# Optimization experiments

Measured on AMD Instinct MI355X. Metric: run time of the kernel, lower is better.

The kernel has to match this reference:

```python
import jax, jax.numpy as jnp
import numpy as np

B, D, M_CONS = 512, 1024, 256
TOL = 0.01          # projection_tolerance
ROUNDS = 3
RHO0 = 3.0          # step
XRHO0 = 0.5         # forward() default xrho
FACTOR = 1.0
MAX_ITER = 30       # cap on the (originally unbounded) Dykstra while-loop


def setup_inputs() -> dict:
    key = jax.random.key(0)
    k1, k2, k3, k4, k5 = jax.random.split(key, 5)
    A = jax.random.normal(k1, (M_CONS, D), jnp.float32) / np.float32(np.sqrt(D))
    # feasible b so the polyhedron {Ax=b, x>=0} is nonempty and Dykstra converges
    x_feas = jax.nn.relu(jax.random.normal(k2, (D,), jnp.float32))
    b = A @ x_feas                                  # [M_CONS]
    AA = A.T @ jnp.linalg.inv(A @ A.T)              # [D, M_CONS], precomputed as in __init__
    c = jax.random.normal(k3, (B, D), jnp.float32)
    L = jax.random.normal(k4, (D, D), jnp.float32)
    Lam = 1.0 + 0.1 * jax.random.normal(k5, (D,), jnp.float32)
    return {"c": c, "A": A, "b": b, "AA": AA, "L": L, "Lam": Lam}


def reference(c, A, b, AA, L, Lam):
    # step matrix: L @ diag(Lam) @ inv(L)   (recomputed identically each round in torch)
    M = (L * Lam[None, :]) @ jnp.linalg.inv(L)      # [D, D]

    def proj(x):  # affine projection onto {Ax = b}: (x.T - AA @ (A x.T - b)).T
        return x - (x @ A.T - b[None, :]) @ AA.T    # [B, D]

    def project_pol(x0):  # Dykstra alternating projection onto {Ax=b} n {x>=0}
        def body(carry, _):
            x, p, q, y_out, done = carry
            y = proj(x + p)
            err = jnp.max(jax.nn.relu(-y))
            y_out = jnp.where(done, y_out, y)       # freeze output at first convergence
            xn = jax.nn.relu(y + q)
            pn = x + p - y
            qn = y + q - xn
            sel = lambda old, new: jnp.where(done, old, new)
            new_done = done | (err < TOL)
            return (sel(x, xn), sel(p, pn), sel(q, qn), y_out, new_done), None

        z = jnp.zeros_like(x0)
        init = (x0, z, z, x0, jnp.array(False))
        (xf, pf, qf, y_out, d), _ = jax.lax.scan(body, init, None, length=MAX_ITER)
        return y_out

    x = jnp.zeros_like(c)
    rho, xrho = RHO0, XRHO0
    for _ in range(ROUNDS):
        x = x - (xrho * (x @ M.T) + rho * c)
        x = project_pol(x)
        rho = rho * FACTOR
        xrho = xrho * FACTOR
    return x
```

## Files before the change

kernel.cpp:

```cpp
#include <hip/hip_runtime.h>

#define D      1024
#define BSZ    512
#define MC     256
#define NBK    64
#define NPAN   16
#define N_ROUNDS 3
#define MAXIT  30
#define TOLV   0.01f
#define RHOV   3.0f
#define XRHOV  0.5f
#define GRID   256
#define NGA    128
#define NGB    128

#define TS   0
#define QS   4096
#define US   8192
#define PART 9216
#define BS   13312
#define RED  13568
#define SMF  13600

struct KArgs {
  const float *c, *A, *b, *AA, *L, *Lam;
  float *yout, *F, *Ybuf, *Wm;
  float *t, *At, *AAt;
  int *perm, *rmap;
  unsigned *slotsF, *slotsG, *errb;
};

__device__ __forceinline__ void fbar(unsigned* slots, int lid, int count, unsigned target) {
  __syncthreads();
  if (threadIdx.x == 0) {
    __builtin_amdgcn_fence(__ATOMIC_RELEASE, "agent");
    __hip_atomic_store(&slots[lid * 16], target, __ATOMIC_RELAXED, __HIP_MEMORY_SCOPE_AGENT);
  }
  for (int i = threadIdx.x; i < count; i += 256)
    while (__hip_atomic_load(&slots[i * 16], __ATOMIC_RELAXED, __HIP_MEMORY_SCOPE_AGENT) < target)
      __builtin_amdgcn_s_sleep(1);
  __builtin_amdgcn_fence(__ATOMIC_ACQUIRE, "agent");
  __syncthreads();
}

__device__ __forceinline__ void tile_fma(const float (*As)[68], const float (*Bs)[68],
                                         float acc[4][4], const int tx, const int ty) {
#pragma unroll 8
  for (int kk = 0; kk < 64; ++kk) {
    const float4 a4 = *(const float4*)(&As[kk][ty * 4]);
    const float4 b4 = *(const float4*)(&Bs[kk][tx * 4]);
    const float a0 = a4.x, a1 = a4.y, a2 = a4.z, a3 = a4.w;
    const float b0 = b4.x, b1 = b4.y, b2 = b4.z, b3 = b4.w;
    acc[0][0] = fmaf(a0, b0, acc[0][0]); acc[0][1] = fmaf(a0, b1, acc[0][1]);
    acc[0][2] = fmaf(a0, b2, acc[0][2]); acc[0][3] = fmaf(a0, b3, acc[0][3]);
    acc[1][0] = fmaf(a1, b0, acc[1][0]); acc[1][1] = fmaf(a1, b1, acc[1][1]);
    acc[1][2] = fmaf(a1, b2, acc[1][2]); acc[1][3] = fmaf(a1, b3, acc[1][3]);
    acc[2][0] = fmaf(a2, b0, acc[2][0]); acc[2][1] = fmaf(a2, b1, acc[2][1]);
    acc[2][2] = fmaf(a2, b2, acc[2][2]); acc[2][3] = fmaf(a2, b3, acc[2][3]);
    acc[3][0] = fmaf(a3, b0, acc[3][0]); acc[3][1] = fmaf(a3, b1, acc[3][1]);
    acc[3][2] = fmaf(a3, b2, acc[3][2]); acc[3][3] = fmaf(a3, b3, acc[3][3]);
  }
}

__device__ void ph_prep(float* sm, int vb, const float* L, const float* Lam,
                        float* F, float* Ybuf) {
  float (*tile)[65] = (float(*)[65])sm;
  const int bi = vb >> 4, bj = vb & 15;
  const int tx = threadIdx.x & 63, ty4 = threadIdx.x >> 6;
  const int i0 = bi * 64, j0 = bj * 64;
  for (int r = ty4; r < 64; r += 4) {
    const float v = L[(size_t)(i0 + r) * D + j0 + tx];
    F[(size_t)(i0 + r) * D + j0 + tx] = v;
    tile[r][tx] = v;
  }
  __syncthreads();
  for (int r = ty4; r < 64; r += 4) {
    const int j = j0 + r;
    Ybuf[(size_t)j * D + i0 + tx] = Lam[j] * tile[tx][r];
  }
  __syncthreads();
}

__device__ void ph_transpose(float* sm, const float* src, float* dst,
                             int srows, int scols, int tr, int tc) {
  float (*tile)[65] = (float(*)[65])sm;
  const int tx = threadIdx.x & 63, ty = threadIdx.x >> 6;
  for (int r = ty; r < 64; r += 4)
    tile[r][tx] = src[(size_t)(tr * 64 + r) * scols + tc * 64 + tx];
  __syncthreads();
  for (int r = ty; r < 64; r += 4)
    dst[(size_t)(tc * 64 + r) * srows + tr * 64 + tx] = tile[tx][r];
  __syncthreads();
}

__device__ void ph_lu_diag(float* sm, float* F, int* perm, int* rmap, int k) {
  float (*blk)[65] = (float(*)[65])sm;
  int* pr_sh = (int*)&sm[8960];
  int* rmp   = (int*)&sm[8964];
  const int tid = threadIdx.x;
  const int c0 = k * NBK;
  for (int e = tid; e < 4096; e += 256) {
    const int r = e >> 6, c = e & 63;
    blk[r][c] = F[(size_t)(c0 + r) * D + c0 + c];
  }
  if (tid < 64) rmp[tid] = tid;
  __syncthreads();
  for (int j = 0; j < 64; ++j) {
    if (tid < 64) {
      float v = (tid >= j) ? fabsf(blk[tid][j]) : -1.0f;
      int ridx = tid;
      for (int off = 32; off > 0; off >>= 1) {
        const float ov = __shfl_down(v, off);
        const int oi = __shfl_down(ridx, off);
        if (ov > v) { v = ov; ridx = oi; }
      }
      if (tid == 0) *pr_sh = ridx;
    }
    __syncthreads();
    const int pr = *pr_sh;
    if (pr != j) {
      if (tid < 64) { const float a = blk[j][tid], b = blk[pr][tid]; blk[j][tid] = b; blk[pr][tid] = a; }
      if (tid == 0) {
        int t = perm[c0 + j]; perm[c0 + j] = perm[c0 + pr]; perm[c0 + pr] = t;
        t = rmp[j]; rmp[j] = rmp[pr]; rmp[pr] = t;
      }
    }
    __syncthreads();
    const float inv = 1.0f / blk[j][j];
    const int r = tid >> 2, l4 = tid & 3;
    if (r > j) {
      const float lval = blk[r][j] * inv;
      if (l4 == 0) blk[r][j] = lval;
      for (int c = j + 1 + l4; c < 64; c += 4)
        blk[r][c] = fmaf(-lval, blk[j][c], blk[r][c]);
    }
    __syncthreads();
  }
  for (int e = tid; e < 4096; e += 256) {
    const int r = e >> 6, c = e & 63;
    F[(size_t)(c0 + r) * D + c0 + c] = blk[r][c];
  }
  if (tid < 64) rmap[tid] = rmp[tid];
  __syncthreads();
}

__device__ void ph_leftperm(float* sm, float* F, const int* rmap, int k, int chunk) {
  float (*tile)[65] = (float(*)[65])sm;
  int* rm = (int*)&sm[8960];
  const int tid = threadIdx.x;
  const int c0 = k * NBK;
  const int col0 = chunk * 64;
  if (tid < 64) rm[tid] = rmap[tid];
  __syncthreads();
  for (int e = tid; e < 4096; e += 256) {
    const int r = e >> 6, c = e & 63;
    tile[r][c] = F[(size_t)(c0 + rm[r]) * D + col0 + c];
  }
  __syncthreads();
  for (int e = tid; e < 4096; e += 256) {
    const int r = e >> 6, c = e & 63;
    F[(size_t)(c0 + r) * D + col0 + c] = tile[r][c];
  }
}

__device__ void ph_l21(float* sm, float* F, int k, int vb) {
  const int c0 = k * NBK;
  const int row0 = c0 + NBK;
  const int nrows = D - row0;
  float (*U)[65] = (float(*)[65])sm;
  const int tid = threadIdx.x;
  for (int e = tid; e < 4096; e += 256) { const int r = e >> 6, c = e & 63; U[r][c] = F[(size_t)(c0 + r) * D + c0 + c]; }
  __syncthreads();
  const int r = vb * 256 + tid;
  if (r >= nrows) return;
  float* Arow = &F[(size_t)(row0 + r) * D + c0];
  float x[64];
#pragma unroll
  for (int i = 0; i < 16; ++i) *(float4*)&x[i * 4] = *(const float4*)&Arow[i * 4];
#pragma unroll
  for (int jj = 0; jj < 64; ++jj) {
    float s0 = 0.f, s1 = 0.f, s2 = 0.f, s3 = 0.f;
#pragma unroll
    for (int i = 0; i + 3 < jj; i += 4) {
      s0 = fmaf(x[i], U[i][jj], s0);
      s1 = fmaf(x[i + 1], U[i + 1][jj], s1);
      s2 = fmaf(x[i + 2], U[i + 2][jj], s2);
      s3 = fmaf(x[i + 3], U[i + 3][jj], s3);
    }
#pragma unroll
    for (int i = (jj / 4) * 4; i < jj; ++i) s0 = fmaf(x[i], U[i][jj], s0);
    const float a = x[jj] - ((s0 + s1) + (s2 + s3));
    x[jj] = a / U[jj][jj];
  }
#pragma unroll
  for (int i = 0; i < 16; ++i) *(float4*)&Arow[i * 4] = *(const float4*)&x[i * 4];
}

__device__ void ph_trsm(float* sm, float* F, const int* rmap, int k, int vb) {
  const int c0 = k * NBK;
  const int colstart = c0 + NBK;
  const int ncols = D - colstart;
  float (*Lw)[65] = (float(*)[65])sm;
  int* rm = (int*)&sm[8960];
  const int tid = threadIdx.x;
  for (int e = tid; e < 4096; e += 256) { const int r = e >> 6, c = e & 63; Lw[r][c] = F[(size_t)(c0 + r) * D + c0 + c]; }
  if (tid < 64) rm[tid] = rmap[tid];
  __syncthreads();
  const int cidx = vb * 256 + tid;
  if (cidx >= ncols) return;
  const int col = colstart + cidx;
  float x[64];
#pragma unroll
  for (int i = 0; i < 64; ++i) x[i] = F[(size_t)(c0 + rm[i]) * D + col];
#pragma unroll
  for (int i = 0; i < 64; ++i) {
    float s0 = 0.f, s1 = 0.f, s2 = 0.f, s3 = 0.f;
#pragma unroll
    for (int j = 0; j + 3 < i; j += 4) {
      s0 = fmaf(Lw[i][j], x[j], s0);
      s1 = fmaf(Lw[i][j + 1], x[j + 1], s1);
      s2 = fmaf(Lw[i][j + 2], x[j + 2], s2);
      s3 = fmaf(Lw[i][j + 3], x[j + 3], s3);
    }
#pragma unroll
    for (int j = (i / 4) * 4; j < i; ++j) s0 = fmaf(Lw[i][j], x[j], s0);
    x[i] = x[i] - ((s0 + s1) + (s2 + s3));
  }
#pragma unroll
  for (int i = 0; i < 64; ++i) F[(size_t)(c0 + i) * D + col] = x[i];
}

__device__ void ph_gemm_nn(float* sm, float* F, int k, int vbx, int vby) {
  const int c0 = k * NBK;
  const int o = c0 + NBK;
  float (*As)[68] = (float(*)[68])sm;
  float (*Bs)[68] = (float(*)[68])&sm[4352];
  const int tid = threadIdx.x;
  const int cc0 = o + vbx * 64;
  const int r0 = o + vby * 64;
  for (int e = tid; e < 4096; e += 256) {
    const int r = e >> 6, c = e & 63;
    As[c][r] = F[(size_t)(r0 + r) * D + c0 + c];
    Bs[r][c] = F[(size_t)(c0 + r) * D + cc0 + c];
  }
  __syncthreads();
  float acc[4][4] = {};
  tile_fma(As, Bs, acc, tid & 15, tid >> 4);
  const int tx = tid & 15, ty = tid >> 4;
  for (int i = 0; i < 4; ++i)
    for (int j = 0; j < 4; ++j)
      F[(size_t)(r0 + ty * 4 + i) * D + cc0 + tx * 4 + j] -= acc[i][j];
  __syncthreads();
}

__device__ void ph_fsolve(float* sm, const float* F, float* Y, int k, int vb) {
  float (*T)[65] = (float(*)[65])sm;
  const int tid = threadIdx.x;
  const int c0 = k * NBK;
  for (int e = tid; e < 4096; e += 256) { const int r = e >> 6, c = e & 63; T[c][r] = F[(size_t)(c0 + r) * D + c0 + c]; }
  __syncthreads();
  const int col = vb * 256 + tid;
  float x[64];
#pragma unroll
  for (int i = 0; i < 64; ++i) x[i] = Y[(size_t)(c0 + i) * D + col];
#pragma unroll
  for (int i = 0; i < 64; ++i) {
    float s0 = 0.f, s1 = 0.f, s2 = 0.f, s3 = 0.f;
#pragma unroll
    for (int j = 0; j + 3 < i; j += 4) {
      s0 = fmaf(T[i][j], x[j], s0);
      s1 = fmaf(T[i][j + 1], x[j + 1], s1);
      s2 = fmaf(T[i][j + 2], x[j + 2], s2);
      s3 = fmaf(T[i][j + 3], x[j + 3], s3);
    }
#pragma unroll
    for (int j = (i / 4) * 4; j < i; ++j) s0 = fmaf(T[i][j], x[j], s0);
    const float a = x[i] - ((s0 + s1) + (s2 + s3));
    x[i] = a / T[i][i];
  }
#pragma unroll
  for (int i = 0; i < 64; ++i) Y[(size_t)(c0 + i) * D + col] = x[i];
  __syncthreads();
}

__device__ void ph_bsolve(float* sm, const float* F, float* Y, int k, int vb) {
  float (*T)[65] = (float(*)[65])sm;
  const int tid = threadIdx.x;
  const int c0 = k * NBK;
  for (int e = tid; e < 4096; e += 256) { const int r = e >> 6, c = e & 63; T[c][r] = F[(size_t)(c0 + r) * D + c0 + c]; }
  __syncthreads();
  const int col = vb * 256 + tid;
  float x[64];
#pragma unroll
  for (int i = 0; i < 64; ++i) x[i] = Y[(size_t)(c0 + i) * D + col];
#pragma unroll
  for (int i = 63; i >= 0; --i) {
    float s0 = 0.f, s1 = 0.f, s2 = 0.f, s3 = 0.f;
#pragma unroll
    for (int j = i + 1; j + 3 < 64; j += 4) {
      s0 = fmaf(T[i][j], x[j], s0);
      s1 = fmaf(T[i][j + 1], x[j + 1], s1);
      s2 = fmaf(T[i][j + 2], x[j + 2], s2);
      s3 = fmaf(T[i][j + 3], x[j + 3], s3);
    }
#pragma unroll
    for (int j = i + 1 + (((63 - i) / 4) * 4); j < 64; ++j) s0 = fmaf(T[i][j], x[j], s0);
    x[i] = x[i] - ((s0 + s1) + (s2 + s3));
  }
#pragma unroll
  for (int i = 0; i < 64; ++i) Y[(size_t)(c0 + i) * D + col] = x[i];
  __syncthreads();
}

__device__ void ph_tn(float* sm, const float* F, float* Y, int k, int rlo, int vbx, int vby) {
  const int c0 = k * NBK;
  float (*As)[68] = (float(*)[68])sm;
  float (*Bs)[68] = (float(*)[68])&sm[4352];
  const int tid = threadIdx.x;
  const int cc0 = vbx * 64;
  const int r0 = rlo + vby * 64;
  for (int e = tid; e < 4096; e += 256) {
    const int r = e >> 6, c = e & 63;
    As[r][c] = F[(size_t)(c0 + r) * D + r0 + c];
    Bs[r][c] = Y[(size_t)(c0 + r) * D + cc0 + c];
  }
  __syncthreads();
  float acc[4][4] = {};
  tile_fma(As, Bs, acc, tid & 15, tid >> 4);
  const int tx = tid & 15, ty = tid >> 4;
  for (int i = 0; i < 4; ++i)
    for (int j = 0; j < 4; ++j)
      Y[(size_t)(r0 + ty * 4 + i) * D + cc0 + tx * 4 + j] -= acc[i][j];
  __syncthreads();
}

__device__ void ph_scatter(const float* Y, float* Wm, const int* perm, int vb) {
  const int i = vb >> 2;
  const int c = (vb & 3) * 256 + threadIdx.x;
  Wm[(size_t)perm[i] * D + c] = Y[(size_t)i * D + c];
}

__device__ void ph_round(float* sm, const float* yout, const float* Wm, const float* cmat,
                         float* t, int vbx, int vby) {
  float (*As)[68] = (float(*)[68])sm;
  float (*Bs)[68] = (float(*)[68])&sm[4352];
  const int tid = threadIdx.x;
  const int i0 = vbx * 64;
  const int b0 = vby * 64;
  float acc[4][4] = {};
  for (int kb = 0; kb < D; kb += 64) {
    for (int e = tid; e < 4096; e += 256) {
      const int r = e >> 6, c = e & 63;
      As[c][r] = yout[(size_t)(b0 + r) * D + kb + c];
      Bs[r][c] = Wm[(size_t)(kb + r) * D + i0 + c];
    }
    __syncthreads();
    tile_fma(As, Bs, acc, tid & 15, tid >> 4);
    __syncthreads();
  }
  const int tx = tid & 15, ty = tid >> 4;
  for (int i = 0; i < 4; ++i)
    for (int j = 0; j < 4; ++j) {
      const int b = b0 + ty * 4 + i, col = i0 + tx * 4 + j;
      const float v = yout[(size_t)b * D + col] - XRHOV * acc[i][j] - RHOV * cmat[(size_t)b * D + col];
      t[(size_t)b * D + col] = v;
    }
  __syncthreads();
}

template <int R>
__device__ void dyk_state_init(float* sm, const KArgs& a, int r0) {
  float4* ts4 = (float4*)(sm + TS);
  float4* qs4 = (float4*)(sm + QS);
  const float4* t4 = (const float4*)(a.t + (size_t)r0 * D);
  for (int e = threadIdx.x; e < R * 256; e += 256) {
    ts4[e] = t4[e];
    qs4[e] = make_float4(0.f, 0.f, 0.f, 0.f);
  }
  sm[BS + threadIdx.x] = a.b[threadIdx.x];
  __syncthreads();
}

template <int R>
__device__ void dyk_iter(float* sm, const KArgs& a, int r0) {
  const int tid = threadIdx.x;
  float* ts = sm + TS;
  float* qs = sm + QS;
  float* us = sm + US;
  float* part = sm + PART;

  const int m4 = tid & 63, ks = tid >> 6;
  const float* AtB = a.At + (size_t)ks * 256 * MC + m4 * 4;
  float4 ua[R];
#pragma unroll
  for (int r = 0; r < R; ++r) ua[r] = make_float4(0.f, 0.f, 0.f, 0.f);
  const int kb = ks * 256;
#pragma unroll 2
  for (int k4 = 0; k4 < 64; ++k4) {
    float tr[R][4];
#pragma unroll
    for (int r = 0; r < R; ++r) *(float4*)tr[r] = *(const float4*)&ts[r * 1024 + kb + k4 * 4];
#pragma unroll
    for (int j = 0; j < 4; ++j) {
      const float4 av = *(const float4*)(AtB + (size_t)(k4 * 4 + j) * MC);
#pragma unroll
      for (int r = 0; r < R; ++r) {
        ua[r].x = fmaf(tr[r][j], av.x, ua[r].x);
        ua[r].y = fmaf(tr[r][j], av.y, ua[r].y);
        ua[r].z = fmaf(tr[r][j], av.z, ua[r].z);
        ua[r].w = fmaf(tr[r][j], av.w, ua[r].w);
      }
    }
  }
#pragma unroll
  for (int r = 0; r < R; ++r) ((float4*)part)[(ks * R + r) * 64 + m4] = ua[r];
  __syncthreads();

  {
    const int m = tid;
#pragma unroll
    for (int r = 0; r < R; ++r)
      us[r * 256 + m] = part[(0 * R + r) * 256 + m] + part[(1 * R + r) * 256 + m] +
                        part[(2 * R + r) * 256 + m] + part[(3 * R + r) * 256 + m] - sm[BS + m];
  }
  __syncthreads();

  float4 ya[R];
#pragma unroll
  for (int r = 0; r < R; ++r) ya[r] = make_float4(0.f, 0.f, 0.f, 0.f);
  const float4* AAB = (const float4*)a.AAt;
#pragma unroll 2
  for (int mi = 0; mi < 64; ++mi) {
    float ur[R][4];
#pragma unroll
    for (int r = 0; r < R; ++r) *(float4*)ur[r] = *(const float4*)&us[r * 256 + mi * 4];
#pragma unroll
    for (int j = 0; j < 4; ++j) {
      const float4 w = AAB[(size_t)(mi * 4 + j) * (D / 4) + tid];
#pragma unroll
      for (int r = 0; r < R; ++r) {
        ya[r].x = fmaf(ur[r][j], w.x, ya[r].x);
        ya[r].y = fmaf(ur[r][j], w.y, ya[r].y);
        ya[r].z = fmaf(ur[r][j], w.z, ya[r].z);
        ya[r].w = fmaf(ur[r][j], w.w, ya[r].w);
      }
    }
  }

  float nmax = 0.f;
#pragma unroll
  for (int r = 0; r < R; ++r) {
    const float4 tv = *(const float4*)&ts[r * 1024 + tid * 4];
    float4 y;
    y.x = tv.x - ya[r].x; y.y = tv.y - ya[r].y;
    y.z = tv.z - ya[r].z; y.w = tv.w - ya[r].w;
    ((float4*)a.yout)[(size_t)(r0 + r) * (D / 4) + tid] = y;
    const float4 qv = *(const float4*)&qs[r * 1024 + tid * 4];
    float4 tn, qn;
    { const float yq = y.x + qv.x, xn = fmaxf(yq, 0.f); tn.x = xn + (tv.x - y.x); qn.x = yq - xn; }
    { const float yq = y.y + qv.y, xn = fmaxf(yq, 0.f); tn.y = xn + (tv.y - y.y); qn.y = yq - xn; }
    { const float yq = y.z + qv.z, xn = fmaxf(yq, 0.f); tn.z = xn + (tv.z - y.z); qn.z = yq - xn; }
    { const float yq = y.w + qv.w, xn = fmaxf(yq, 0.f); tn.w = xn + (tv.w - y.w); qn.w = yq - xn; }
    *(float4*)&ts[r * 1024 + tid * 4] = tn;
    *(float4*)&qs[r * 1024 + tid * 4] = qn;
    nmax = fmaxf(nmax, -y.x); nmax = fmaxf(nmax, -y.y);
    nmax = fmaxf(nmax, -y.z); nmax = fmaxf(nmax, -y.w);
  }
#pragma unroll
  for (int off = 32; off > 0; off >>= 1) nmax = fmaxf(nmax, __shfl_down(nmax, off));
  if ((tid & 63) == 0) sm[RED + (tid >> 6)] = nmax;
  __syncthreads();
}

template <int R>
__device__ void dyk_round(float* sm, const KArgs& a, int bid, int nblk, int base) {
  const int r0 = bid * R;
  dyk_state_init<R>(sm, a, r0);
  for (int it = 0; it < MAXIT; ++it) {
    dyk_iter<R>(sm, a, r0);
    if (threadIdx.x == 0) {
      const float bmax = fmaxf(fmaxf(sm[RED], sm[RED + 1]), fmaxf(sm[RED + 2], sm[RED + 3]));
      __hip_atomic_store(&a.errb[(size_t)(base + it) * GRID + bid],
                         __float_as_uint(bmax) | 0x80000000u,
                         __ATOMIC_RELAXED, __HIP_MEMORY_SCOPE_AGENT);
    }
    float v = 0.f;
    if (threadIdx.x < nblk) {
      unsigned u = __hip_atomic_load(&a.errb[(size_t)(base + it) * GRID + threadIdx.x],
                                     __ATOMIC_RELAXED, __HIP_MEMORY_SCOPE_AGENT);
      while (!(u & 0x80000000u)) {
        __builtin_amdgcn_s_sleep(1);
        u = __hip_atomic_load(&a.errb[(size_t)(base + it) * GRID + threadIdx.x],
                              __ATOMIC_RELAXED, __HIP_MEMORY_SCOPE_AGENT);
      }
      v = __uint_as_float(u & 0x7FFFFFFFu);
    }
#pragma unroll
    for (int off = 32; off > 0; off >>= 1) v = fmaxf(v, __shfl_down(v, off));
    __syncthreads();
    if ((threadIdx.x & 63) == 0) sm[RED + (threadIdx.x >> 6)] = v;
    __syncthreads();
    const float gmax = fmaxf(fmaxf(sm[RED], sm[RED + 1]), fmaxf(sm[RED + 2], sm[RED + 3]));
    __syncthreads();
    if (gmax < TOLV) break;
  }
}

__global__ __launch_bounds__(256, 1) void mega(KArgs a) {
  __shared__ alignas(16) float sm[SMF];
  const int bid = blockIdx.x;
  const int tid = threadIdx.x;
  unsigned genF = 0, genG = 0;

  {
    const int gtid = bid * 256 + tid;
    for (int i = gtid; i < BSZ * D; i += GRID * 256) a.t[i] = -RHOV * a.c[i];
    if (gtid < D) a.perm[gtid] = gtid;
  }
  for (int vb = bid; vb < 384; vb += GRID) {
    if (vb < 256) ph_prep(sm, vb, a.L, a.Lam, a.F, a.Ybuf);
    else if (vb < 320) { const int tt = vb - 256; ph_transpose(sm, a.A, a.At, MC, D, tt & 3, tt >> 2); }
    else { const int tt = vb - 320; ph_transpose(sm, a.AA, a.AAt, D, MC, tt & 15, tt >> 4); }
  }
  fbar(a.slotsF, bid, GRID, ++genF);

  if (bid < NGA) {
    dyk_round<4>(sm, a, bid, NGA, 0);
    fbar(a.slotsF, bid, GRID, ++genF);
  } else {
    unsigned* slotsB = a.slotsG + NGB * 16;
    const int vbid = bid - NGA;
    for (int k = 0; k < NPAN; ++k) {
      if (vbid == 0) ph_lu_diag(sm, a.F, a.perm, a.rmap, k);
      fbar(slotsB, vbid, NGB, ++genG);
      const int rem = D - (k + 1) * NBK;
      const int nvb = (rem > 0) ? (rem + 255) / 256 : 0;
      const int ntask = k + 2 * nvb;
      for (int vb = vbid; vb < ntask; vb += NGB) {
        if (vb < k) ph_leftperm(sm, a.F, a.rmap, k, vb);
        else if (vb < k + nvb) ph_l21(sm, a.F, k, vb - k);
        else ph_trsm(sm, a.F, a.rmap, k, vb - k - nvb);
      }
      fbar(slotsB, vbid, NGB, ++genG);
      if (rem > 0) {
        const int nt = rem / 64;
        for (int vb = vbid; vb < nt * nt; vb += NGB) ph_gemm_nn(sm, a.F, k, vb % nt, vb / nt);
        fbar(slotsB, vbid, NGB, ++genG);
      }
    }
    for (int k = 0; k < NPAN; ++k) {
      for (int vb = vbid; vb < 4; vb += NGB) ph_fsolve(sm, a.F, a.Ybuf, k, vb);
      fbar(slotsB, vbid, NGB, ++genG);
      const int rem = D - (k + 1) * NBK;
      if (rem > 0) {
        for (int vb = vbid; vb < 16 * (rem / 64); vb += NGB)
          ph_tn(sm, a.F, a.Ybuf, k, (k + 1) * NBK, vb & 15, vb >> 4);
        fbar(slotsB, vbid, NGB, ++genG);
      }
    }
    for (int k = NPAN - 1; k >= 0; --k) {
      for (int vb = vbid; vb < 4; vb += NGB) ph_bsolve(sm, a.F, a.Ybuf, k, vb);
      fbar(slotsB, vbid, NGB, ++genG);
      if (k > 0) {
        for (int vb = vbid; vb < 16 * k; vb += NGB)
          ph_tn(sm, a.F, a.Ybuf, k, 0, vb & 15, vb >> 4);
        fbar(slotsB, vbid, NGB, ++genG);
      }
    }
    for (int vb = vbid; vb < 4 * D; vb += NGB) ph_scatter(a.Ybuf, a.Wm, a.perm, vb);
    fbar(a.slotsF, bid, GRID, ++genF);
  }

  for (int r = 1; r < N_ROUNDS; ++r) {
    if (bid < 128) ph_round(sm, a.yout, a.Wm, a.c, a.t, bid & 15, bid >> 4);
    fbar(a.slotsF, bid, GRID, ++genF);
    dyk_round<2>(sm, a, bid, GRID, r * MAXIT);
    if (r + 1 < N_ROUNDS)
      fbar(a.slotsF, bid, GRID, ++genF);
  }
}

extern "C" void kernel_launch(void* const* d_in, const int* in_sizes, int n_in,
                              void* d_out, int out_size, void* d_ws, size_t ws_size,
                              hipStream_t stream) {
  (void)in_sizes; (void)n_in; (void)out_size; (void)ws_size;
  KArgs a;
  a.c   = (const float*)d_in[0];
  a.A   = (const float*)d_in[1];
  a.b   = (const float*)d_in[2];
  a.AA  = (const float*)d_in[3];
  a.L   = (const float*)d_in[4];
  a.Lam = (const float*)d_in[5];
  a.yout = (float*)d_out;

  char* w = (char*)d_ws;
  a.slotsF = (unsigned*)w;
  a.slotsG = (unsigned*)(w + 16384);
  a.errb   = (unsigned*)(w + 32768);
  a.rmap   = (int*)(w + 124928);
  w += 131072;
  a.F    = (float*)w; w += (size_t)D * D * 4;
  a.Ybuf = (float*)w; w += (size_t)D * D * 4;
  a.Wm   = (float*)w; w += (size_t)D * D * 4;
  a.t    = (float*)w; w += (size_t)BSZ * D * 4;
  a.At   = (float*)w; w += (size_t)D * MC * 4;
  a.AAt  = (float*)w; w += (size_t)MC * D * 4;
  a.perm = (int*)w;   w += (size_t)D * 4;

  hipMemsetAsync(d_ws, 0, 131072, stream);
  mega<<<dim3(GRID), dim3(256), 0, stream>>>(a);
}
```

Measured before the change: 5.864 ms.

## Replace barrier-heavy triangular solves with per-block column solves and fuse LU diag

Each of the 128 factorization blocks now owns 8 right-hand-side columns and runs the whole forward and backward substitution plus the permutation scatter locally. This removes the many grid-wide barriers of the old panel-parallel fsolve/tn/bsolve schedule. The diagonal LU factorization of the next panel is folded into the GEMM step, so each panel loses one barrier; this needs per-panel rmap storage. Block roles are swapped, and the later Dykstra rounds run on 128 blocks with 4 rows each instead of 256 blocks with 2. In exchange, only 8 threads per block do the serial triangular work, each block re-reads most of F, and half the grid sits idle during the later projection rounds.

```diff
diff --git a/kernel.cpp b/kernel.cpp
--- a/kernel.cpp
+++ b/kernel.cpp
@@ -11,8 +11,8 @@
 #define RHOV   3.0f
 #define XRHOV  0.5f
 #define GRID   256
+#define NGB    128
 #define NGA    128
-#define NGB    128
 
 #define TS   0
 #define QS   4096
@@ -93,7 +93,7 @@
   __syncthreads();
 }
 
-__device__ void ph_lu_diag(float* sm, float* F, int* perm, int* rmap, int k) {
+__device__ void ph_lu_diag(float* sm, float* F, int* perm, int* rmapk, int k) {
   float (*blk)[65] = (float(*)[65])sm;
   int* pr_sh = (int*)&sm[8960];
   int* rmp   = (int*)&sm[8964];
@@ -140,17 +140,17 @@
     const int r = e >> 6, c = e & 63;
     F[(size_t)(c0 + r) * D + c0 + c] = blk[r][c];
   }
-  if (tid < 64) rmap[tid] = rmp[tid];
-  __syncthreads();
-}
-
-__device__ void ph_leftperm(float* sm, float* F, const int* rmap, int k, int chunk) {
+  if (tid < 64) rmapk[tid] = rmp[tid];
+  __syncthreads();
+}
+
+__device__ void ph_leftperm(float* sm, float* F, const int* rmapk, int k, int chunk) {
   float (*tile)[65] = (float(*)[65])sm;
   int* rm = (int*)&sm[8960];
   const int tid = threadIdx.x;
   const int c0 = k * NBK;
   const int col0 = chunk * 64;
-  if (tid < 64) rm[tid] = rmap[tid];
+  if (tid < 64) rm[tid] = rmapk[tid];
   __syncthreads();
   for (int e = tid; e < 4096; e += 256) {
     const int r = e >> 6, c = e & 63;
@@ -196,7 +196,7 @@
   for (int i = 0; i < 16; ++i) *(float4*)&Arow[i * 4] = *(const float4*)&x[i * 4];
 }
 
-__device__ void ph_trsm(float* sm, float* F, const int* rmap, int k, int vb) {
+__device__ void ph_trsm(float* sm, float* F, const int* rmapk, int k, int vb) {
   const int c0 = k * NBK;
   const int colstart = c0 + NBK;
   const int ncols = D - colstart;
@@ -204,7 +204,7 @@
   int* rm = (int*)&sm[8960];
   const int tid = threadIdx.x;
   for (int e = tid; e < 4096; e += 256) { const int r = e >> 6, c = e & 63; Lw[r][c] = F[(size_t)(c0 + r) * D + c0 + c]; }
-  if (tid < 64) rm[tid] = rmap[tid];
+  if (tid < 64) rm[tid] = rmapk[tid];
   __syncthreads();
   const int cidx = vb * 256 + tid;
   if (cidx >= ncols) return;
@@ -253,91 +253,110 @@
   __syncthreads();
 }
 
-__device__ void ph_fsolve(float* sm, const float* F, float* Y, int k, int vb) {
+__device__ void ph_colsolve(float* sm, const KArgs& a, int blk) {
+  const int tid = threadIdx.x;
+  const int col0 = blk * 8;
   float (*T)[65] = (float(*)[65])sm;
-  const int tid = threadIdx.x;
-  const int c0 = k * NBK;
-  for (int e = tid; e < 4096; e += 256) { const int r = e >> 6, c = e & 63; T[c][r] = F[(size_t)(c0 + r) * D + c0 + c]; }
-  __syncthreads();
-  const int col = vb * 256 + tid;
-  float x[64];
-#pragma unroll
-  for (int i = 0; i < 64; ++i) x[i] = Y[(size_t)(c0 + i) * D + col];
-#pragma unroll
-  for (int i = 0; i < 64; ++i) {
-    float s0 = 0.f, s1 = 0.f, s2 = 0.f, s3 = 0.f;
-#pragma unroll
-    for (int j = 0; j + 3 < i; j += 4) {
-      s0 = fmaf(T[i][j], x[j], s0);
-      s1 = fmaf(T[i][j + 1], x[j + 1], s1);
-      s2 = fmaf(T[i][j + 2], x[j + 2], s2);
-      s3 = fmaf(T[i][j + 3], x[j + 3], s3);
-    }
-#pragma unroll
-    for (int j = (i / 4) * 4; j < i; ++j) s0 = fmaf(T[i][j], x[j], s0);
-    const float a = x[i] - ((s0 + s1) + (s2 + s3));
-    x[i] = a / T[i][i];
-  }
-#pragma unroll
-  for (int i = 0; i < 64; ++i) Y[(size_t)(c0 + i) * D + col] = x[i];
-  __syncthreads();
-}
-
-__device__ void ph_bsolve(float* sm, const float* F, float* Y, int k, int vb) {
-  float (*T)[65] = (float(*)[65])sm;
-  const int tid = threadIdx.x;
-  const int c0 = k * NBK;
-  for (int e = tid; e < 4096; e += 256) { const int r = e >> 6, c = e & 63; T[c][r] = F[(size_t)(c0 + r) * D + c0 + c]; }
-  __syncthreads();
-  const int col = vb * 256 + tid;
-  float x[64];
-#pragma unroll
-  for (int i = 0; i < 64; ++i) x[i] = Y[(size_t)(c0 + i) * D + col];
-#pragma unroll
-  for (int i = 63; i >= 0; --i) {
-    float s0 = 0.f, s1 = 0.f, s2 = 0.f, s3 = 0.f;
-#pragma unroll
-    for (int j = i + 1; j + 3 < 64; j += 4) {
-      s0 = fmaf(T[i][j], x[j], s0);
-      s1 = fmaf(T[i][j + 1], x[j + 1], s1);
-      s2 = fmaf(T[i][j + 2], x[j + 2], s2);
-      s3 = fmaf(T[i][j + 3], x[j + 3], s3);
-    }
-#pragma unroll
-    for (int j = i + 1 + (((63 - i) / 4) * 4); j < 64; ++j) s0 = fmaf(T[i][j], x[j], s0);
-    x[i] = x[i] - ((s0 + s1) + (s2 + s3));
-  }
-#pragma unroll
-  for (int i = 0; i < 64; ++i) Y[(size_t)(c0 + i) * D + col] = x[i];
-  __syncthreads();
-}
-
-__device__ void ph_tn(float* sm, const float* F, float* Y, int k, int rlo, int vbx, int vby) {
-  const int c0 = k * NBK;
-  float (*As)[68] = (float(*)[68])sm;
-  float (*Bs)[68] = (float(*)[68])&sm[4352];
-  const int tid = threadIdx.x;
-  const int cc0 = vbx * 64;
-  const int r0 = rlo + vby * 64;
-  for (int e = tid; e < 4096; e += 256) {
-    const int r = e >> 6, c = e & 63;
-    As[r][c] = F[(size_t)(c0 + r) * D + r0 + c];
-    Bs[r][c] = Y[(size_t)(c0 + r) * D + cc0 + c];
-  }
-  __syncthreads();
-  float acc[4][4] = {};
-  tile_fma(As, Bs, acc, tid & 15, tid >> 4);
-  const int tx = tid & 15, ty = tid >> 4;
-  for (int i = 0; i < 4; ++i)
-    for (int j = 0; j < 4; ++j)
-      Y[(size_t)(r0 + ty * 4 + i) * D + cc0 + tx * 4 + j] -= acc[i][j];
-  __syncthreads();
-}
-
-__device__ void ph_scatter(const float* Y, float* Wm, const int* perm, int vb) {
-  const int i = vb >> 2;
-  const int c = (vb & 3) * 256 + threadIdx.x;
-  Wm[(size_t)perm[i] * D + c] = Y[(size_t)i * D + c];
+  float* xs = sm + 4160;
+  const int colT = tid & 7, r2 = tid >> 3;
+  for (int k = 0; k < NPAN; ++k) {
+    const int c0 = k * NBK;
+    __threadfence_block();
+    __syncthreads();
+    for (int e = tid; e < 4096; e += 256) { const int r = e >> 6, c = e & 63; T[c][r] = a.F[(size_t)(c0 + r) * D + c0 + c]; }
+    __syncthreads();
+    if (tid < 8) {
+      const int col = col0 + tid;
+      float x[64];
+#pragma unroll
+      for (int i = 0; i < 64; ++i) x[i] = a.Ybuf[(size_t)(c0 + i) * D + col];
+#pragma unroll
+      for (int i = 0; i < 64; ++i) {
+        float s0 = 0.f, s1 = 0.f, s2 = 0.f, s3 = 0.f;
+#pragma unroll
+        for (int j = 0; j + 3 < i; j += 4) {
+          s0 = fmaf(T[i][j], x[j], s0);
+          s1 = fmaf(T[i][j + 1], x[j + 1], s1);
+          s2 = fmaf(T[i][j + 2], x[j + 2], s2);
+          s3 = fmaf(T[i][j + 3], x[j + 3], s3);
+        }
+#pragma unroll
+        for (int j = (i / 4) * 4; j < i; ++j) s0 = fmaf(T[i][j], x[j], s0);
+        const float v = x[i] - ((s0 + s1) + (s2 + s3));
+        x[i] = v / T[i][i];
+      }
+#pragma unroll
+      for (int i = 0; i < 64; ++i) { a.Ybuf[(size_t)(c0 + i) * D + col] = x[i]; xs[i * 8 + tid] = x[i]; }
+    }
+    __syncthreads();
+    for (int rb = c0 + NBK; rb < D; rb += NBK) {
+      const int rr = r2 * 2;
+      float s0 = 0.f, s1 = 0.f, t0 = 0.f, t1 = 0.f;
+#pragma unroll
+      for (int j = 0; j < 64; j += 2) {
+        const float2 f0 = *(const float2*)&a.F[(size_t)(c0 + j) * D + rb + rr];
+        const float2 f1 = *(const float2*)&a.F[(size_t)(c0 + j + 1) * D + rb + rr];
+        const float xa = xs[j * 8 + colT], xb = xs[(j + 1) * 8 + colT];
+        s0 = fmaf(f0.x, xa, s0); t0 = fmaf(f0.y, xa, t0);
+        s1 = fmaf(f1.x, xb, s1); t1 = fmaf(f1.y, xb, t1);
+      }
+      a.Ybuf[(size_t)(rb + rr) * D + col0 + colT]     -= (s0 + s1);
+      a.Ybuf[(size_t)(rb + rr + 1) * D + col0 + colT] -= (t0 + t1);
+    }
+  }
+  for (int k = NPAN - 1; k >= 0; --k) {
+    const int c0 = k * NBK;
+    __threadfence_block();
+    __syncthreads();
+    for (int e = tid; e < 4096; e += 256) { const int r = e >> 6, c = e & 63; T[c][r] = a.F[(size_t)(c0 + r) * D + c0 + c]; }
+    __syncthreads();
+    if (tid < 8) {
+      const int col = col0 + tid;
+      float x[64];
+#pragma unroll
+      for (int i = 0; i < 64; ++i) x[i] = a.Ybuf[(size_t)(c0 + i) * D + col];
+#pragma unroll
+      for (int i = 63; i >= 0; --i) {
+        float s0 = 0.f, s1 = 0.f, s2 = 0.f, s3 = 0.f;
+#pragma unroll
+        for (int j = i + 1; j + 3 < 64; j += 4) {
+          s0 = fmaf(T[i][j], x[j], s0);
+          s1 = fmaf(T[i][j + 1], x[j + 1], s1);
+          s2 = fmaf(T[i][j + 2], x[j + 2], s2);
+          s3 = fmaf(T[i][j + 3], x[j + 3], s3);
+        }
+#pragma unroll
+        for (int j = i + 1 + (((63 - i) / 4) * 4); j < 64; ++j) s0 = fmaf(T[i][j], x[j], s0);
+        x[i] = x[i] - ((s0 + s1) + (s2 + s3));
+      }
+#pragma unroll
+      for (int i = 0; i < 64; ++i) { a.Ybuf[(size_t)(c0 + i) * D + col] = x[i]; xs[i * 8 + tid] = x[i]; }
+    }
+    __syncthreads();
+    for (int rb = 0; rb < c0; rb += NBK) {
+      const int rr = r2 * 2;
+      float s0 = 0.f, s1 = 0.f, t0 = 0.f, t1 = 0.f;
+#pragma unroll
+      for (int j = 0; j < 64; j += 2) {
+        const float2 f0 = *(const float2*)&a.F[(size_t)(c0 + j) * D + rb + rr];
+        const float2 f1 = *(const float2*)&a.F[(size_t)(c0 + j + 1) * D + rb + rr];
+        const float xa = xs[j * 8 + colT], xb = xs[(j + 1) * 8 + colT];
+        s0 = fmaf(f0.x, xa, s0); t0 = fmaf(f0.y, xa, t0);
+        s1 = fmaf(f1.x, xb, s1); t1 = fmaf(f1.y, xb, t1);
+      }
+      a.Ybuf[(size_t)(rb + rr) * D + col0 + colT]     -= (s0 + s1);
+      a.Ybuf[(size_t)(rb + rr + 1) * D + col0 + colT] -= (t0 + t1);
+    }
+  }
+  __threadfence_block();
+  __syncthreads();
+  for (int i = tid; i < D; i += 256) {
+    const int dst = a.perm[i];
+    const float4 v0 = *(const float4*)&a.Ybuf[(size_t)i * D + col0];
+    const float4 v1 = *(const float4*)&a.Ybuf[(size_t)i * D + col0 + 4];
+    *(float4*)&a.Wm[(size_t)dst * D + col0] = v0;
+    *(float4*)&a.Wm[(size_t)dst * D + col0 + 4] = v1;
+  }
 }
 
 __device__ void ph_round(float* sm, const float* yout, const float* Wm, const float* cmat,
@@ -473,14 +492,14 @@
 }
 
 template <int R>
-__device__ void dyk_round(float* sm, const KArgs& a, int bid, int nblk, int base) {
-  const int r0 = bid * R;
+__device__ void dyk_round(float* sm, const KArgs& a, int lid, int nblk, int base) {
+  const int r0 = lid * R;
   dyk_state_init<R>(sm, a, r0);
   for (int it = 0; it < MAXIT; ++it) {
     dyk_iter<R>(sm, a, r0);
     if (threadIdx.x == 0) {
       const float bmax = fmaxf(fmaxf(sm[RED], sm[RED + 1]), fmaxf(sm[RED + 2], sm[RED + 3]));
-      __hip_atomic_store(&a.errb[(size_t)(base + it) * GRID + bid],
+      __hip_atomic_store(&a.errb[(size_t)(base + it) * GRID + lid],
                          __float_as_uint(bmax) | 0x80000000u,
                          __ATOMIC_RELAXED, __HIP_MEMORY_SCOPE_AGENT);
     }
@@ -522,61 +541,49 @@
     else if (vb < 320) { const int tt = vb - 256; ph_transpose(sm, a.A, a.At, MC, D, tt & 3, tt >> 2); }
     else { const int tt = vb - 320; ph_transpose(sm, a.AA, a.AAt, D, MC, tt & 15, tt >> 4); }
   }
+  if (bid == 0) {
+    __threadfence_block();
+    __syncthreads();
+    ph_lu_diag(sm, a.F, a.perm, a.rmap, 0);
+  }
   fbar(a.slotsF, bid, GRID, ++genF);
 
-  if (bid < NGA) {
-    dyk_round<4>(sm, a, bid, NGA, 0);
-    fbar(a.slotsF, bid, GRID, ++genF);
-  } else {
-    unsigned* slotsB = a.slotsG + NGB * 16;
-    const int vbid = bid - NGA;
+  if (bid < NGB) {
+    unsigned* slotsB = a.slotsG;
+    const int vbid = bid;
     for (int k = 0; k < NPAN; ++k) {
-      if (vbid == 0) ph_lu_diag(sm, a.F, a.perm, a.rmap, k);
-      fbar(slotsB, vbid, NGB, ++genG);
       const int rem = D - (k + 1) * NBK;
       const int nvb = (rem > 0) ? (rem + 255) / 256 : 0;
       const int ntask = k + 2 * nvb;
       for (int vb = vbid; vb < ntask; vb += NGB) {
-        if (vb < k) ph_leftperm(sm, a.F, a.rmap, k, vb);
+        if (vb < k) ph_leftperm(sm, a.F, a.rmap + k * 64, k, vb);
         else if (vb < k + nvb) ph_l21(sm, a.F, k, vb - k);
-        else ph_trsm(sm, a.F, a.rmap, k, vb - k - nvb);
+        else ph_trsm(sm, a.F, a.rmap + k * 64, k, vb - k - nvb);
       }
       fbar(slotsB, vbid, NGB, ++genG);
       if (rem > 0) {
         const int nt = rem / 64;
         for (int vb = vbid; vb < nt * nt; vb += NGB) ph_gemm_nn(sm, a.F, k, vb % nt, vb / nt);
+        if (vbid == 0 && k + 1 < NPAN) {
+          __threadfence_block();
+          __syncthreads();
+          ph_lu_diag(sm, a.F, a.perm, a.rmap + (k + 1) * 64, k + 1);
+        }
         fbar(slotsB, vbid, NGB, ++genG);
       }
     }
-    for (int k = 0; k < NPAN; ++k) {
-      for (int vb = vbid; vb < 4; vb += NGB) ph_fsolve(sm, a.F, a.Ybuf, k, vb);
-      fbar(slotsB, vbid, NGB, ++genG);
-      const int rem = D - (k + 1) * NBK;
-      if (rem > 0) {
-        for (int vb = vbid; vb < 16 * (rem / 64); vb += NGB)
-          ph_tn(sm, a.F, a.Ybuf, k, (k + 1) * NBK, vb & 15, vb >> 4);
-        fbar(slotsB, vbid, NGB, ++genG);
-      }
-    }
-    for (int k = NPAN - 1; k >= 0; --k) {
-      for (int vb = vbid; vb < 4; vb += NGB) ph_bsolve(sm, a.F, a.Ybuf, k, vb);
-      fbar(slotsB, vbid, NGB, ++genG);
-      if (k > 0) {
-        for (int vb = vbid; vb < 16 * k; vb += NGB)
-          ph_tn(sm, a.F, a.Ybuf, k, 0, vb & 15, vb >> 4);
-        fbar(slotsB, vbid, NGB, ++genG);
-      }
-    }
-    for (int vb = vbid; vb < 4 * D; vb += NGB) ph_scatter(a.Ybuf, a.Wm, a.perm, vb);
+    ph_colsolve(sm, a, vbid);
     fbar(a.slotsF, bid, GRID, ++genF);
+  } else {
+    dyk_round<4>(sm, a, bid - NGB, NGA, 0);
+    fbar(a.slotsF, bid, GRID, ++genF);
   }
 
   for (int r = 1; r < N_ROUNDS; ++r) {
-    if (bid < 128) ph_round(sm, a.yout, a.Wm, a.c, a.t, bid & 15, bid >> 4);
+    if (bid >= NGB) ph_round(sm, a.yout, a.Wm, a.c, a.t, (bid - NGB) & 15, (bid - NGB) >> 4);
     fbar(a.slotsF, bid, GRID, ++genF);
-    dyk_round<2>(sm, a, bid, GRID, r * MAXIT);
-    if (r + 1 < N_ROUNDS)
-      fbar(a.slotsF, bid, GRID, ++genF);
+    if (bid >= NGB) dyk_round<4>(sm, a, bid - NGB, NGA, r * MAXIT);
+    if (r + 1 < N_ROUNDS) fbar(a.slotsF, bid, GRID, ++genF);
   }
 }
 
```

New measurement: 6.508 ms. +11.0%, slower.

## Double grid, look ahead panel LU diagonal, and rebalance Dykstra/LU block groups

Applied to the files above, without the earlier changes.

Doubles the persistent grid to 512 blocks at two blocks per CU, giving the LU factorisation group and the first Dykstra group 256 blocks each. The next panel's diagonal LU is now factored by block 0 right after its own trailing-GEMM tile. That tile is the one the diagonal depends on, so this removes one grid barrier per panel. Each panel keeps its own row map so the lookahead does not overwrite the map still in use. Later Dykstra rounds run on 128 blocks with four rows each instead of the whole grid, and the spin-wait sleep is lengthened. The trade-offs are heavier barrier traffic over twice as many blocks and a larger zeroed workspace.

```diff
diff --git a/kernel.cpp b/kernel.cpp
--- a/kernel.cpp
+++ b/kernel.cpp
@@ -10,9 +10,9 @@
 #define TOLV   0.01f
 #define RHOV   3.0f
 #define XRHOV  0.5f
-#define GRID   256
-#define NGA    128
-#define NGB    128
+#define GRID   512
+#define NGB    256
+#define NGA    256
 
 #define TS   0
 #define QS   4096
@@ -38,7 +38,7 @@
   }
   for (int i = threadIdx.x; i < count; i += 256)
     while (__hip_atomic_load(&slots[i * 16], __ATOMIC_RELAXED, __HIP_MEMORY_SCOPE_AGENT) < target)
-      __builtin_amdgcn_s_sleep(1);
+      __builtin_amdgcn_s_sleep(2);
   __builtin_amdgcn_fence(__ATOMIC_ACQUIRE, "agent");
   __syncthreads();
 }
@@ -93,7 +93,7 @@
   __syncthreads();
 }
 
-__device__ void ph_lu_diag(float* sm, float* F, int* perm, int* rmap, int k) {
+__device__ void ph_lu_diag(float* sm, float* F, int* perm, int* rmapk, int k) {
   float (*blk)[65] = (float(*)[65])sm;
   int* pr_sh = (int*)&sm[8960];
   int* rmp   = (int*)&sm[8964];
@@ -140,17 +140,17 @@
     const int r = e >> 6, c = e & 63;
     F[(size_t)(c0 + r) * D + c0 + c] = blk[r][c];
   }
-  if (tid < 64) rmap[tid] = rmp[tid];
-  __syncthreads();
-}
-
-__device__ void ph_leftperm(float* sm, float* F, const int* rmap, int k, int chunk) {
+  if (tid < 64) rmapk[tid] = rmp[tid];
+  __syncthreads();
+}
+
+__device__ void ph_leftperm(float* sm, float* F, const int* rmapk, int k, int chunk) {
   float (*tile)[65] = (float(*)[65])sm;
   int* rm = (int*)&sm[8960];
   const int tid = threadIdx.x;
   const int c0 = k * NBK;
   const int col0 = chunk * 64;
-  if (tid < 64) rm[tid] = rmap[tid];
+  if (tid < 64) rm[tid] = rmapk[tid];
   __syncthreads();
   for (int e = tid; e < 4096; e += 256) {
     const int r = e >> 6, c = e & 63;
@@ -196,7 +196,7 @@
   for (int i = 0; i < 16; ++i) *(float4*)&Arow[i * 4] = *(const float4*)&x[i * 4];
 }
 
-__device__ void ph_trsm(float* sm, float* F, const int* rmap, int k, int vb) {
+__device__ void ph_trsm(float* sm, float* F, const int* rmapk, int k, int vb) {
   const int c0 = k * NBK;
   const int colstart = c0 + NBK;
   const int ncols = D - colstart;
@@ -204,7 +204,7 @@
   int* rm = (int*)&sm[8960];
   const int tid = threadIdx.x;
   for (int e = tid; e < 4096; e += 256) { const int r = e >> 6, c = e & 63; Lw[r][c] = F[(size_t)(c0 + r) * D + c0 + c]; }
-  if (tid < 64) rm[tid] = rmap[tid];
+  if (tid < 64) rm[tid] = rmapk[tid];
   __syncthreads();
   const int cidx = vb * 256 + tid;
   if (cidx >= ncols) return;
@@ -473,14 +473,14 @@
 }
 
 template <int R>
-__device__ void dyk_round(float* sm, const KArgs& a, int bid, int nblk, int base) {
-  const int r0 = bid * R;
+__device__ void dyk_round(float* sm, const KArgs& a, int lid, int nblk, int base) {
+  const int r0 = lid * R;
   dyk_state_init<R>(sm, a, r0);
   for (int it = 0; it < MAXIT; ++it) {
     dyk_iter<R>(sm, a, r0);
     if (threadIdx.x == 0) {
       const float bmax = fmaxf(fmaxf(sm[RED], sm[RED + 1]), fmaxf(sm[RED + 2], sm[RED + 3]));
-      __hip_atomic_store(&a.errb[(size_t)(base + it) * GRID + bid],
+      __hip_atomic_store(&a.errb[(size_t)(base + it) * GRID + lid],
                          __float_as_uint(bmax) | 0x80000000u,
                          __ATOMIC_RELAXED, __HIP_MEMORY_SCOPE_AGENT);
     }
@@ -506,7 +506,7 @@
   }
 }
 
-__global__ __launch_bounds__(256, 1) void mega(KArgs a) {
+__global__ __launch_bounds__(256, 2) void mega(KArgs a) {
   __shared__ alignas(16) float sm[SMF];
   const int bid = blockIdx.x;
   const int tid = threadIdx.x;
@@ -522,29 +522,34 @@
     else if (vb < 320) { const int tt = vb - 256; ph_transpose(sm, a.A, a.At, MC, D, tt & 3, tt >> 2); }
     else { const int tt = vb - 320; ph_transpose(sm, a.AA, a.AAt, D, MC, tt & 15, tt >> 4); }
   }
+  if (bid == 0) {
+    __threadfence_block();
+    __syncthreads();
+    ph_lu_diag(sm, a.F, a.perm, a.rmap, 0);
+  }
   fbar(a.slotsF, bid, GRID, ++genF);
 
-  if (bid < NGA) {
-    dyk_round<4>(sm, a, bid, NGA, 0);
-    fbar(a.slotsF, bid, GRID, ++genF);
-  } else {
-    unsigned* slotsB = a.slotsG + NGB * 16;
-    const int vbid = bid - NGA;
+  if (bid < NGB) {
+    unsigned* slotsB = a.slotsG;
+    const int vbid = bid;
     for (int k = 0; k < NPAN; ++k) {
-      if (vbid == 0) ph_lu_diag(sm, a.F, a.perm, a.rmap, k);
-      fbar(slotsB, vbid, NGB, ++genG);
       const int rem = D - (k + 1) * NBK;
       const int nvb = (rem > 0) ? (rem + 255) / 256 : 0;
       const int ntask = k + 2 * nvb;
       for (int vb = vbid; vb < ntask; vb += NGB) {
-        if (vb < k) ph_leftperm(sm, a.F, a.rmap, k, vb);
+        if (vb < k) ph_leftperm(sm, a.F, a.rmap + k * 64, k, vb);
         else if (vb < k + nvb) ph_l21(sm, a.F, k, vb - k);
-        else ph_trsm(sm, a.F, a.rmap, k, vb - k - nvb);
+        else ph_trsm(sm, a.F, a.rmap + k * 64, k, vb - k - nvb);
       }
       fbar(slotsB, vbid, NGB, ++genG);
       if (rem > 0) {
         const int nt = rem / 64;
         for (int vb = vbid; vb < nt * nt; vb += NGB) ph_gemm_nn(sm, a.F, k, vb % nt, vb / nt);
+        if (vbid == 0 && k + 1 < NPAN) {
+          __threadfence_block();
+          __syncthreads();
+          ph_lu_diag(sm, a.F, a.perm, a.rmap + (k + 1) * 64, k + 1);
+        }
         fbar(slotsB, vbid, NGB, ++genG);
       }
     }
@@ -569,14 +574,16 @@
     }
     for (int vb = vbid; vb < 4 * D; vb += NGB) ph_scatter(a.Ybuf, a.Wm, a.perm, vb);
     fbar(a.slotsF, bid, GRID, ++genF);
+  } else {
+    dyk_round<2>(sm, a, bid - NGB, NGA, 0);
+    fbar(a.slotsF, bid, GRID, ++genF);
   }
 
   for (int r = 1; r < N_ROUNDS; ++r) {
     if (bid < 128) ph_round(sm, a.yout, a.Wm, a.c, a.t, bid & 15, bid >> 4);
     fbar(a.slotsF, bid, GRID, ++genF);
-    dyk_round<2>(sm, a, bid, GRID, r * MAXIT);
-    if (r + 1 < N_ROUNDS)
-      fbar(a.slotsF, bid, GRID, ++genF);
+    if (bid >= NGB && bid < NGB + 128) dyk_round<4>(sm, a, bid - NGB, 128, r * MAXIT);
+    if (r + 1 < N_ROUNDS) fbar(a.slotsF, bid, GRID, ++genF);
   }
 }
 
@@ -595,10 +602,10 @@
 
   char* w = (char*)d_ws;
   a.slotsF = (unsigned*)w;
-  a.slotsG = (unsigned*)(w + 16384);
-  a.errb   = (unsigned*)(w + 32768);
-  a.rmap   = (int*)(w + 124928);
-  w += 131072;
+  a.slotsG = (unsigned*)(w + 32768);
+  a.errb   = (unsigned*)(w + 49152);
+  a.rmap   = (int*)(w + 233472);
+  w += 237568;
   a.F    = (float*)w; w += (size_t)D * D * 4;
   a.Ybuf = (float*)w; w += (size_t)D * D * 4;
   a.Wm   = (float*)w; w += (size_t)D * D * 4;
@@ -607,6 +614,6 @@
   a.AAt  = (float*)w; w += (size_t)MC * D * 4;
   a.perm = (int*)w;   w += (size_t)D * 4;
 
-  hipMemsetAsync(d_ws, 0, 131072, stream);
+  hipMemsetAsync(d_ws, 0, 237568, stream);
   mega<<<dim3(GRID), dim3(256), 0, stream>>>(a);
 }
```

Result: slower. 6.688 ms (+14.1%).
